# Kernel tuning notes

Hardware: AMD Instinct MI355X
Metric: run time of the kernel (lower is better)

## Reference

```python
import jax, jax.numpy as jnp
import numpy as np

N = 4096
INPUT_SIZE = 768
DICT_SIZE = 16384
TOP_K = 64


def setup_inputs() -> dict:
    key = jax.random.key(0)
    k1, k2, k3 = jax.random.split(key, 3)
    x = jax.random.normal(k1, (N, INPUT_SIZE), dtype=jnp.float32)
    W_enc = jax.random.normal(k2, (INPUT_SIZE, DICT_SIZE), dtype=jnp.float32) * (1.0 / np.sqrt(INPUT_SIZE))
    b_enc = jax.random.normal(k3, (DICT_SIZE,), dtype=jnp.float32) * 0.01
    return {"x": x, "W_enc": W_enc, "b_enc": b_enc, "top_k": TOP_K}


def reference(x, W_enc, b_enc, top_k):
    # pre_acts = relu(x @ W + b): [N, dict_size]
    pre_acts = jax.nn.relu(jnp.matmul(x, W_enc) + b_enc)
    flat = pre_acts.reshape(-1)  # [N * dict_size]
    k = top_k * x.shape[0]       # global batch-wise budget
    vals, idx = jax.lax.top_k(flat, k)
    out = jnp.zeros_like(flat).at[idx].set(vals)
    return out.reshape(pre_acts.shape)
```

## Files before the change

kernel.cpp:

```cpp
#include <hip/hip_runtime.h>

#define N_ROWS 4096
#define K_DIM  768
#define M_DIM  16384
#define TOTAL  (N_ROWS * M_DIM)
#define K_SEL  262144u
#define NB     8192
#define CAP    8192
#define LOWBITS 0x3F800000u

#define BM 128
#define BN 128
#define BK 32

__global__ __launch_bounds__(256) void gemm_relu(const float* __restrict__ A,
                                                 const float* __restrict__ B,
                                                 const float* __restrict__ bias,
                                                 float* __restrict__ C) {
    __shared__ float As[BK][BM + 1];
    __shared__ float Bs[BK][BN];

    const int tid = threadIdx.x;
    const int wid = tid >> 6;
    const int lane = tid & 63;
    const int tx = tid & 15;
    const int ty = tid >> 4;
    const int row0 = blockIdx.y * BM;
    const int col0 = blockIdx.x * BN;

    float acc[8][8];
#pragma unroll
    for (int i = 0; i < 8; ++i)
#pragma unroll
        for (int j = 0; j < 8; ++j) acc[i][j] = 0.f;

    float4 areg[4];
#pragma unroll
    for (int L = 0; L < 4; ++L) {
        int f = tid + L * 256;
        int r = f >> 3, c4 = (f & 7) << 2;
        areg[L] = *(const float4*)&A[(long long)(row0 + r) * K_DIM + c4];
    }

    for (int k0 = 0; k0 < K_DIM; k0 += BK) {
#pragma unroll
        for (int q = 0; q < 4; ++q) {
            int r = wid * 8 + q * 2 + (lane >> 5);
            const float* src = &B[(long long)(k0 + r) * M_DIM + col0 + ((lane & 31) << 2)];
            __builtin_amdgcn_global_load_lds(
                (const __attribute__((address_space(1))) void*)src,
                (__attribute__((address_space(3))) void*)&Bs[wid * 8 + q * 2][0],
                16, 0, 0);
        }
#pragma unroll
        for (int L = 0; L < 4; ++L) {
            int f = tid + L * 256;
            int r = f >> 3, c4 = (f & 7) << 2;
            As[c4 + 0][r] = areg[L].x; As[c4 + 1][r] = areg[L].y;
            As[c4 + 2][r] = areg[L].z; As[c4 + 3][r] = areg[L].w;
        }
        __syncthreads();

        if (k0 + BK < K_DIM) {
#pragma unroll
            for (int L = 0; L < 4; ++L) {
                int f = tid + L * 256;
                int r = f >> 3, c4 = (f & 7) << 2;
                areg[L] = *(const float4*)&A[(long long)(row0 + r) * K_DIM + (k0 + BK) + c4];
            }
        }

#pragma unroll
        for (int kk = 0; kk < BK; ++kk) {
            float a8[8], b8[8];
#pragma unroll
            for (int i = 0; i < 8; ++i) a8[i] = As[kk][(ty << 3) + i];
#pragma unroll
            for (int j = 0; j < 8; ++j) b8[j] = Bs[kk][tx + (j << 4)];
#pragma unroll
            for (int i = 0; i < 8; ++i)
#pragma unroll
                for (int j = 0; j < 8; ++j) acc[i][j] = fmaf(a8[i], b8[j], acc[i][j]);
        }
        __syncthreads();
    }

#pragma unroll
    for (int i = 0; i < 8; ++i) {
        long long row = row0 + (ty << 3) + i;
#pragma unroll
        for (int j = 0; j < 8; ++j) {
            float v = acc[i][j] + bias[col0 + tx + (j << 4)];
            C[row * M_DIM + col0 + tx + (j << 4)] = fmaxf(v, 0.f);
        }
    }
}


__global__ __launch_bounds__(256) void hist1_kernel(const float4* __restrict__ out4,
                                                    unsigned* __restrict__ hist) {
    __shared__ unsigned h[NB];
    for (int i = threadIdx.x; i < NB; i += 256) h[i] = 0u;
    __syncthreads();
    const int stride = gridDim.x * 256;
    for (int i = blockIdx.x * 256 + threadIdx.x; i < TOTAL / 4; i += stride) {
        float4 v = out4[i];
        unsigned b;
        b = __float_as_uint(v.x); if (b >= LOWBITS) atomicAdd(&h[b >> 18], 1u);
        b = __float_as_uint(v.y); if (b >= LOWBITS) atomicAdd(&h[b >> 18], 1u);
        b = __float_as_uint(v.z); if (b >= LOWBITS) atomicAdd(&h[b >> 18], 1u);
        b = __float_as_uint(v.w); if (b >= LOWBITS) atomicAdd(&h[b >> 18], 1u);
    }
    __syncthreads();
    for (int i = threadIdx.x; i < NB; i += 256)
        if (h[i]) atomicAdd(&hist[i], h[i]);
}

__global__ __launch_bounds__(1024) void select_kernel(const unsigned* __restrict__ hist,
                                                      unsigned* __restrict__ meta, int mode) {
    __shared__ unsigned ssum[1024];
    const int t = threadIdx.x;
    const unsigned target = (mode == 0) ? K_SEL : meta[1];
    unsigned loc[8];
    unsigned s = 0;
    const int base = t * 8;
#pragma unroll
    for (int j = 0; j < 8; ++j) { loc[j] = hist[base + j]; s += loc[j]; }
    ssum[t] = s;
    __syncthreads();
    for (int off = 1; off < 1024; off <<= 1) {
        unsigned v = ssum[t];
        unsigned a = (t + off < 1024) ? ssum[t + off] : 0u;
        __syncthreads();
        ssum[t] = v + a;
        __syncthreads();
    }
    const unsigned suffix_excl = ssum[t] - s;
    unsigned cum = suffix_excl;
    for (int j = 7; j >= 0; --j) {
        unsigned Sb1 = cum;
        cum += loc[j];
        if (cum >= target && Sb1 < target) {
            if (mode == 0) { meta[0] = (unsigned)(base + j); meta[1] = target - Sb1; }
            else           { meta[2] = (unsigned)(base + j); meta[3] = target - Sb1; }
        }
    }
}

__global__ __launch_bounds__(256) void hist2_kernel(const float4* __restrict__ out4,
                                                    const unsigned* __restrict__ meta,
                                                    unsigned* __restrict__ hist) {
    __shared__ unsigned h[NB];
    for (int i = threadIdx.x; i < NB; i += 256) h[i] = 0u;
    __syncthreads();
    const unsigned B0 = meta[0];
    const int stride = gridDim.x * 256;
    for (int i = blockIdx.x * 256 + threadIdx.x; i < TOTAL / 4; i += stride) {
        float4 v = out4[i];
        unsigned b;
        b = __float_as_uint(v.x); if ((b >> 18) == B0) atomicAdd(&h[(b >> 5) & 8191u], 1u);
        b = __float_as_uint(v.y); if ((b >> 18) == B0) atomicAdd(&h[(b >> 5) & 8191u], 1u);
        b = __float_as_uint(v.z); if ((b >> 18) == B0) atomicAdd(&h[(b >> 5) & 8191u], 1u);
        b = __float_as_uint(v.w); if ((b >> 18) == B0) atomicAdd(&h[(b >> 5) & 8191u], 1u);
    }
    __syncthreads();
    for (int i = threadIdx.x; i < NB; i += 256)
        if (h[i]) atomicAdd(&hist[i], h[i]);
}

__global__ __launch_bounds__(256) void collect_kernel(const float4* __restrict__ out4,
                                                      unsigned* __restrict__ meta,
                                                      float* __restrict__ cvals,
                                                      unsigned* __restrict__ cidx) {
    const unsigned B0 = meta[0];
    const unsigned B1 = meta[2];
    const int stride = gridDim.x * 256;
    for (int i = blockIdx.x * 256 + threadIdx.x; i < TOTAL / 4; i += stride) {
        float4 v = out4[i];
        const float* vp = &v.x;
#pragma unroll
        for (int j = 0; j < 4; ++j) {
            unsigned b = __float_as_uint(vp[j]);
            if ((b >> 18) == B0 && ((b >> 5) & 8191u) == B1) {
                unsigned p = atomicAdd(&meta[6], 1u);
                if (p < CAP) { cvals[p] = vp[j]; cidx[p] = (unsigned)(i * 4 + j); }
            }
        }
    }
}

__global__ __launch_bounds__(256) void finalize_kernel(const float* __restrict__ cvals,
                                                       const unsigned* __restrict__ cidx,
                                                       unsigned* __restrict__ meta) {
    __shared__ unsigned cnt[32];
    __shared__ unsigned sh_cnt, sh_l, sh_t, sh_prefix;
    __shared__ int sh_lo, sh_hi;
    const int t = threadIdx.x;
    unsigned m = meta[6]; if (m > CAP) m = CAP;
    const unsigned rem2 = meta[3];
    if (t < 32) cnt[t] = 0u;
    __syncthreads();
    for (unsigned i = t; i < m; i += 256) {
        unsigned b = __float_as_uint(cvals[i]);
        atomicAdd(&cnt[b & 31u], 1u);
        if (i == 0) sh_prefix = b & ~31u;
    }
    __syncthreads();
    if (t == 0) {
        unsigned suf = 0; int l = 31;
        for (; l > 0; --l) { if (suf + cnt[l] >= rem2) break; suf += cnt[l]; }
        sh_l = (unsigned)l;
        sh_t = rem2 - suf;
        meta[4] = sh_prefix | (unsigned)l;
        sh_lo = -1; sh_hi = TOTAL - 1;
    }
    __syncthreads();
    const unsigned l = sh_l, tneed = sh_t;
    for (int it = 0; it < 28; ++it) {
        __syncthreads();
        int lo = sh_lo, hi = sh_hi;
        if (lo + 1 < hi) {
            int mid = lo + ((hi - lo) >> 1);
            if (t == 0) sh_cnt = 0u;
            __syncthreads();
            unsigned c = 0;
            for (unsigned i = t; i < m; i += 256) {
                unsigned b = __float_as_uint(cvals[i]);
                if ((b & 31u) == l && cidx[i] <= (unsigned)mid) ++c;
            }
            if (c) atomicAdd(&sh_cnt, c);
            __syncthreads();
            if (t == 0) { if (sh_cnt >= tneed) sh_hi = mid; else sh_lo = mid; }
        }
    }
    __syncthreads();
    if (t == 0) meta[8] = (unsigned)sh_hi;
}

__global__ __launch_bounds__(256) void apply_kernel(float4* __restrict__ out4,
                                                    const unsigned* __restrict__ meta) {
    const unsigned tau = meta[4];
    const unsigned cut = meta[8];
    const int stride = gridDim.x * 256;
    for (int i = blockIdx.x * 256 + threadIdx.x; i < TOTAL / 4; i += stride) {
        float4 v = out4[i];
        unsigned idx0 = (unsigned)i * 4u;
        unsigned b;
        b = __float_as_uint(v.x); if (!(b > tau || (b == tau && idx0 + 0u <= cut))) v.x = 0.f;
        b = __float_as_uint(v.y); if (!(b > tau || (b == tau && idx0 + 1u <= cut))) v.y = 0.f;
        b = __float_as_uint(v.z); if (!(b > tau || (b == tau && idx0 + 2u <= cut))) v.z = 0.f;
        b = __float_as_uint(v.w); if (!(b > tau || (b == tau && idx0 + 3u <= cut))) v.w = 0.f;
        out4[i] = v;
    }
}

extern "C" void kernel_launch(void* const* d_in, const int* in_sizes, int n_in,
                              void* d_out, int out_size, void* d_ws, size_t ws_size,
                              hipStream_t stream) {
    const float* x    = (const float*)d_in[0];
    const float* Wenc = (const float*)d_in[1];
    const float* benc = (const float*)d_in[2];
    float* out = (float*)d_out;

    unsigned char* ws = (unsigned char*)d_ws;
    unsigned* hist1 = (unsigned*)ws;
    unsigned* hist2 = (unsigned*)(ws + 32768);
    unsigned* meta  = (unsigned*)(ws + 65536);
    float*    cvals = (float*)(ws + 65792);
    unsigned* cidx  = (unsigned*)(ws + 65792 + CAP * 4);

    hipMemsetAsync(d_ws, 0, 65792, stream);

    gemm_relu<<<dim3(M_DIM / BN, N_ROWS / BM), 256, 0, stream>>>(x, Wenc, benc, out);

    hist1_kernel<<<2048, 256, 0, stream>>>((const float4*)out, hist1);
    select_kernel<<<1, 1024, 0, stream>>>(hist1, meta, 0);
    hist2_kernel<<<2048, 256, 0, stream>>>((const float4*)out, meta, hist2);
    select_kernel<<<1, 1024, 0, stream>>>(hist2, meta, 1);
    collect_kernel<<<2048, 256, 0, stream>>>((const float4*)out, meta, cvals, cidx);
    finalize_kernel<<<1, 256, 0, stream>>>(cvals, cidx, meta);
    apply_kernel<<<2048, 256, 0, stream>>>((float4*)out, meta);
}
```

Before: 1.839 ms.

## Enlarge GEMM block tile to 256x128 with 16x8 per-thread register tiles

Doubles the row tile of the GEMM so each thread computes a 16x8 accumulator block, reading A and B from shared memory as float4 vectors and writing output with float4 stores. This raises arithmetic intensity per shared-memory load and halves the number of blocks re-reading B. It increases register use (more accumulators and staged A registers), which can lower occupancy or cause spills, and changes LDS padding to keep vector alignment.

New measurement: 1.640 ms. 10.8% less time.

```diff
diff --git a/kernel.cpp b/kernel.cpp
--- a/kernel.cpp
+++ b/kernel.cpp
@@ -9,15 +9,16 @@
 #define CAP    8192
 #define LOWBITS 0x3F800000u
 
-#define BM 128
+#define BM 256
 #define BN 128
 #define BK 32
+#define APAD 4
 
 __global__ __launch_bounds__(256) void gemm_relu(const float* __restrict__ A,
                                                  const float* __restrict__ B,
                                                  const float* __restrict__ bias,
                                                  float* __restrict__ C) {
-    __shared__ float As[BK][BM + 1];
+    __shared__ float As[BK][BM + APAD];
     __shared__ float Bs[BK][BN];
 
     const int tid = threadIdx.x;
@@ -28,15 +29,15 @@
     const int row0 = blockIdx.y * BM;
     const int col0 = blockIdx.x * BN;
 
-    float acc[8][8];
-#pragma unroll
-    for (int i = 0; i < 8; ++i)
+    float acc[16][8];
+#pragma unroll
+    for (int i = 0; i < 16; ++i)
 #pragma unroll
         for (int j = 0; j < 8; ++j) acc[i][j] = 0.f;
 
-    float4 areg[4];
-#pragma unroll
-    for (int L = 0; L < 4; ++L) {
+    float4 areg[8];
+#pragma unroll
+    for (int L = 0; L < 8; ++L) {
         int f = tid + L * 256;
         int r = f >> 3, c4 = (f & 7) << 2;
         areg[L] = *(const float4*)&A[(long long)(row0 + r) * K_DIM + c4];
@@ -53,7 +54,7 @@
                 16, 0, 0);
         }
 #pragma unroll
-        for (int L = 0; L < 4; ++L) {
+        for (int L = 0; L < 8; ++L) {
             int f = tid + L * 256;
             int r = f >> 3, c4 = (f & 7) << 2;
             As[c4 + 0][r] = areg[L].x; As[c4 + 1][r] = areg[L].y;
@@ -63,36 +64,48 @@
 
         if (k0 + BK < K_DIM) {
 #pragma unroll
-            for (int L = 0; L < 4; ++L) {
+            for (int L = 0; L < 8; ++L) {
                 int f = tid + L * 256;
                 int r = f >> 3, c4 = (f & 7) << 2;
                 areg[L] = *(const float4*)&A[(long long)(row0 + r) * K_DIM + (k0 + BK) + c4];
             }
         }
 
-#pragma unroll
+#pragma unroll 4
         for (int kk = 0; kk < BK; ++kk) {
-            float a8[8], b8[8];
-#pragma unroll
-            for (int i = 0; i < 8; ++i) a8[i] = As[kk][(ty << 3) + i];
-#pragma unroll
-            for (int j = 0; j < 8; ++j) b8[j] = Bs[kk][tx + (j << 4)];
-#pragma unroll
-            for (int i = 0; i < 8; ++i)
-#pragma unroll
-                for (int j = 0; j < 8; ++j) acc[i][j] = fmaf(a8[i], b8[j], acc[i][j]);
-        }
-        __syncthreads();
-    }
-
-#pragma unroll
-    for (int i = 0; i < 8; ++i) {
-        long long row = row0 + (ty << 3) + i;
-#pragma unroll
-        for (int j = 0; j < 8; ++j) {
-            float v = acc[i][j] + bias[col0 + tx + (j << 4)];
-            C[row * M_DIM + col0 + tx + (j << 4)] = fmaxf(v, 0.f);
-        }
+            float4 a0 = *(const float4*)&As[kk][(ty << 4) + 0];
+            float4 a1 = *(const float4*)&As[kk][(ty << 4) + 4];
+            float4 a2 = *(const float4*)&As[kk][(ty << 4) + 8];
+            float4 a3 = *(const float4*)&As[kk][(ty << 4) + 12];
+            float4 b0 = *(const float4*)&Bs[kk][tx << 2];
+            float4 b1 = *(const float4*)&Bs[kk][64 + (tx << 2)];
+            float av[16] = {a0.x, a0.y, a0.z, a0.w, a1.x, a1.y, a1.z, a1.w,
+                            a2.x, a2.y, a2.z, a2.w, a3.x, a3.y, a3.z, a3.w};
+            float bv[8]  = {b0.x, b0.y, b0.z, b0.w, b1.x, b1.y, b1.z, b1.w};
+#pragma unroll
+            for (int i = 0; i < 16; ++i)
+#pragma unroll
+                for (int j = 0; j < 8; ++j) acc[i][j] = fmaf(av[i], bv[j], acc[i][j]);
+        }
+        __syncthreads();
+    }
+
+    float bv[8];
+#pragma unroll
+    for (int j = 0; j < 4; ++j) {
+        bv[j]     = bias[col0 + (tx << 2) + j];
+        bv[4 + j] = bias[col0 + 64 + (tx << 2) + j];
+    }
+#pragma unroll
+    for (int i = 0; i < 16; ++i) {
+        long long row = row0 + (ty << 4) + i;
+        float4 o0, o1;
+        o0.x = fmaxf(acc[i][0] + bv[0], 0.f); o0.y = fmaxf(acc[i][1] + bv[1], 0.f);
+        o0.z = fmaxf(acc[i][2] + bv[2], 0.f); o0.w = fmaxf(acc[i][3] + bv[3], 0.f);
+        o1.x = fmaxf(acc[i][4] + bv[4], 0.f); o1.y = fmaxf(acc[i][5] + bv[5], 0.f);
+        o1.z = fmaxf(acc[i][6] + bv[6], 0.f); o1.w = fmaxf(acc[i][7] + bv[7], 0.f);
+        *(float4*)&C[row * M_DIM + col0 + (tx << 2)] = o0;
+        *(float4*)&C[row * M_DIM + col0 + 64 + (tx << 2)] = o1;
     }
 }
 
```
